# Performance work log

Measured on AMD Instinct MI355X. Metric: run time of the kernel, lower is better.

Reference implementation:

```python
import jax, jax.numpy as jnp
import numpy as np

N_NODES = 100000
N_EDGES = 1600000
D_IN = 128
D_OUT = 128


def setup_inputs() -> dict:
    key = jax.random.key(0)
    k1, k2, k3, k4 = jax.random.split(key, 4)
    feat = jax.random.normal(k1, (N_NODES, D_IN), dtype=jnp.float32)
    W1 = jax.random.normal(k2, (D_OUT, D_IN), dtype=jnp.float32) * (1.0 / np.sqrt(D_IN))
    src = jax.random.randint(k3, (N_EDGES,), 0, N_NODES, dtype=jnp.int32)
    # ensure every dst node has at least one in-edge (no empty segments, like a
    # DGL graph without isolated destination nodes)
    dst_rand = jax.random.randint(k4, (N_EDGES - N_NODES,), 0, N_NODES, dtype=jnp.int32)
    dst = jnp.concatenate([jnp.arange(N_NODES, dtype=jnp.int32), dst_rand])
    return {"feat": feat, "W1": W1, "src": src, "dst": dst}


def reference(feat, W1, src, dst):
    # nn.Linear(bias=False): h = feat @ W1.T   -> [N, D_OUT]
    norm_h = jnp.einsum("nd,od->no", feat, W1)
    # copy_u message + max reduce: segment-max of projected src feats onto dst
    msgs = norm_h[src]                                   # [E, D_OUT] gather
    h_N = jax.ops.segment_max(msgs, dst, num_segments=feat.shape[0])  # [N, D_OUT]
    # concat(feat_dst, h_N) along feature dim
    return jnp.concatenate([feat, h_N], axis=1)          # [N, D_IN + D_OUT]
```

## Files before the change

kernel.cpp:

```cpp
#include <hip/hip_runtime.h>
#include <hip/hip_bf16.h>
#include <cfloat>

typedef short bf16x8 __attribute__((ext_vector_type(8)));
typedef float f32x4 __attribute__((ext_vector_type(4)));

constexpr int NB_PAD  = 800;
constexpr int PCHUNK  = 8192;
constexpr int NCH_MAX = 200;
constexpr int OFFROW  = 804;
constexpr int BCAPM   = 4096;

__device__ __forceinline__ unsigned short f32_to_bf16_rne(float f) {
    unsigned int u = __float_as_uint(f);
    u += 0x7fffu + ((u >> 16) & 1u);
    return (unsigned short)(u >> 16);
}
__device__ __forceinline__ float b2f(unsigned int w, int k) {
    return (float)((int)(w << (24 - 8 * k)) >> 24);
}

__global__ __launch_bounds__(256) void ka_part_gemm_kernel(
    const float* __restrict__ feat, const float* __restrict__ W1,
    signed char* __restrict__ norm8, float* __restrict__ rowscale,
    float* __restrict__ out,
    const int* __restrict__ src, const int* __restrict__ dst,
    int* __restrict__ part, unsigned short* __restrict__ offRow,
    int N, int E, int nb, int partBlocks) {
    __shared__ __align__(16) char smem[38912];
    const int t = threadIdx.x;

    if ((int)blockIdx.x < partBlocks) {
        int* stage   = (int*)smem;
        int* pkCnt   = stage + PCHUNK;
        int* pkOff   = pkCnt + 400;
        int* pkLoc   = pkOff + 400;
        int* partial = pkLoc + 400;

        const int c0 = blockIdx.x * PCHUNK;
        const int n  = (E - c0 < PCHUNK) ? (E - c0) : PCHUNK;

        for (int i = t; i < 400; i += 256) pkCnt[i] = 0;
        __syncthreads();

#pragma unroll
        for (int j = 0; j < PCHUNK / 1024; ++j) {
            int i = (j * 256 + t) * 4;
            if (i + 3 < n) {
                int4 d4 = *(const int4*)(dst + c0 + i);
                atomicAdd(&pkCnt[(d4.x >> 7) >> 1], 1 << (((d4.x >> 7) & 1) << 4));
                atomicAdd(&pkCnt[(d4.y >> 7) >> 1], 1 << (((d4.y >> 7) & 1) << 4));
                atomicAdd(&pkCnt[(d4.z >> 7) >> 1], 1 << (((d4.z >> 7) & 1) << 4));
                atomicAdd(&pkCnt[(d4.w >> 7) >> 1], 1 << (((d4.w >> 7) & 1) << 4));
            } else if (i < n) {
                for (int k = i; k < n; ++k) {
                    int b = dst[c0 + k] >> 7;
                    atomicAdd(&pkCnt[b >> 1], 1 << ((b & 1) << 4));
                }
            }
        }
        __syncthreads();

        {
            int w0 = 0, w1 = 0;
            if (t < 200) { w0 = pkCnt[2 * t]; w1 = pkCnt[2 * t + 1]; }
            int c0_ = w0 & 0xFFFF, c1_ = (w0 >> 16) & 0xFFFF;
            int c2_ = w1 & 0xFFFF, c3_ = (w1 >> 16) & 0xFFFF;
            partial[t] = c0_ + c1_ + c2_ + c3_;
            __syncthreads();
            for (int d = 1; d < 256; d <<= 1) {
                int x = (t >= d) ? partial[t - d] : 0;
                __syncthreads();
                if (t >= d) partial[t] += x;
                __syncthreads();
            }
            if (t < 200) {
                int run = t ? partial[t - 1] : 0;
                int o0 = run, o1 = o0 + c0_, o2 = o1 + c1_, o3 = o2 + c2_;
                pkOff[2 * t]     = o0 | (o1 << 16);
                pkOff[2 * t + 1] = o2 | (o3 << 16);
                pkLoc[2 * t]     = o0 | (o1 << 16);
                pkLoc[2 * t + 1] = o2 | (o3 << 16);
            }
        }
        __syncthreads();

#pragma unroll
        for (int j = 0; j < PCHUNK / 1024; ++j) {
            int i = (j * 256 + t) * 4;
            if (i + 3 < n) {
                int4 d4 = *(const int4*)(dst + c0 + i);
                int4 s4 = *(const int4*)(src + c0 + i);
                int b, sh, old;
                b = d4.x >> 7; sh = (b & 1) << 4;
                old = atomicAdd(&pkLoc[b >> 1], 1 << sh);
                stage[(old >> sh) & 0xFFFF] = s4.x | ((d4.x & 127) << 17);
                b = d4.y >> 7; sh = (b & 1) << 4;
                old = atomicAdd(&pkLoc[b >> 1], 1 << sh);
                stage[(old >> sh) & 0xFFFF] = s4.y | ((d4.y & 127) << 17);
                b = d4.z >> 7; sh = (b & 1) << 4;
                old = atomicAdd(&pkLoc[b >> 1], 1 << sh);
                stage[(old >> sh) & 0xFFFF] = s4.z | ((d4.z & 127) << 17);
                b = d4.w >> 7; sh = (b & 1) << 4;
                old = atomicAdd(&pkLoc[b >> 1], 1 << sh);
                stage[(old >> sh) & 0xFFFF] = s4.w | ((d4.w & 127) << 17);
            } else if (i < n) {
                for (int k = i; k < n; ++k) {
                    int d = dst[c0 + k];
                    int b = d >> 7, sh = (b & 1) << 4;
                    int old = atomicAdd(&pkLoc[b >> 1], 1 << sh);
                    stage[(old >> sh) & 0xFFFF] = src[c0 + k] | ((d & 127) << 17);
                }
            }
        }
        __syncthreads();

        for (int i = t * 4; i < n; i += 1024) {
            if (i + 3 < n) *(int4*)(part + c0 + i) = *(const int4*)(stage + i);
            else for (int k = i; k < n; ++k) part[c0 + k] = stage[k];
        }
        unsigned short* orow = offRow + (size_t)blockIdx.x * OFFROW;
        for (int b = t; b <= nb; b += 256)
            orow[b] = (unsigned short)((pkOff[b >> 1] >> ((b & 1) << 4)) & 0xFFFF);
    } else {
        unsigned short* smW = (unsigned short*)smem;
#pragma unroll
        for (int i = 0; i < 8; ++i) {
            int f = i * 256 + t;
            int l = f & 63, kb = (f >> 6) & 3, ot = f >> 8;
            int wrow = ot * 16 + (l & 15);
            int k0 = kb * 32 + (l >> 4) * 8;
            const float* p = W1 + wrow * 128 + k0;
            float4 f0 = *(const float4*)p;
            float4 f1 = *(const float4*)(p + 4);
            union { unsigned short h[8]; uint4 v; } pk;
            pk.h[0] = f32_to_bf16_rne(f0.x); pk.h[1] = f32_to_bf16_rne(f0.y);
            pk.h[2] = f32_to_bf16_rne(f0.z); pk.h[3] = f32_to_bf16_rne(f0.w);
            pk.h[4] = f32_to_bf16_rne(f1.x); pk.h[5] = f32_to_bf16_rne(f1.y);
            pk.h[6] = f32_to_bf16_rne(f1.z); pk.h[7] = f32_to_bf16_rne(f1.w);
            *(uint4*)(smW + (size_t)f * 8) = pk.v;
        }

        const int bid = blockIdx.x - partBlocks;
        const int w = t >> 6;
        const int l = t & 63;
        const int brow0 = bid * 64;
        const int row = brow0 + w * 16 + (l & 15);
        const int kq = (l >> 4) * 8;
        const bool valid = row < N;

        bf16x8 a[4];
        const float* fr = feat + (size_t)row * 128;
        float* orow_ = out + (size_t)row * 256;
#pragma unroll
        for (int kb = 0; kb < 4; ++kb) {
            float4 f0 = make_float4(0.f, 0.f, 0.f, 0.f), f1 = f0;
            if (valid) {
                f0 = *(const float4*)(fr + kb * 32 + kq);
                f1 = *(const float4*)(fr + kb * 32 + kq + 4);
                *(float4*)(orow_ + kb * 32 + kq) = f0;
                *(float4*)(orow_ + kb * 32 + kq + 4) = f1;
            }
            bf16x8 av;
            av[0] = (short)f32_to_bf16_rne(f0.x); av[1] = (short)f32_to_bf16_rne(f0.y);
            av[2] = (short)f32_to_bf16_rne(f0.z); av[3] = (short)f32_to_bf16_rne(f0.w);
            av[4] = (short)f32_to_bf16_rne(f1.x); av[5] = (short)f32_to_bf16_rne(f1.y);
            av[6] = (short)f32_to_bf16_rne(f1.z); av[7] = (short)f32_to_bf16_rne(f1.w);
            a[kb] = av;
        }
        __syncthreads();

        const bf16x8* bfr = (const bf16x8*)smem;
        f32x4 zero = {0.f, 0.f, 0.f, 0.f};
        f32x4 acc[8];
#pragma unroll
        for (int ot = 0; ot < 8; ++ot) acc[ot] = zero;
#pragma unroll
        for (int ot = 0; ot < 8; ++ot) {
#pragma unroll
            for (int kb = 0; kb < 4; ++kb) {
                bf16x8 b = bfr[(ot * 4 + kb) * 64 + l];
                acc[ot] = __builtin_amdgcn_mfma_f32_16x16x32_bf16(a[kb], b, acc[ot], 0, 0, 0);
            }
        }

        const int r0 = w * 16 + (l >> 4) * 4;
        float inv[4], scl[4];
#pragma unroll
        for (int j = 0; j < 4; ++j) {
            float am = 0.f;
#pragma unroll
            for (int ot = 0; ot < 8; ++ot) am = fmaxf(am, __builtin_fabsf(acc[ot][j]));
#pragma unroll
            for (int d = 1; d < 16; d <<= 1) am = fmaxf(am, __shfl_xor(am, d, 64));
            am = fmaxf(am, 1e-30f);
            inv[j] = 127.0f / am;
            scl[j] = am * (1.0f / 127.0f);
        }
        if ((l & 15) == 0) {
#pragma unroll
            for (int j = 0; j < 4; ++j) {
                int grow = brow0 + r0 + j;
                if (grow < N) rowscale[grow] = scl[j];
            }
        }
        __syncthreads();

        char (*sm8)[144] = (char (*)[144])smem;
        const int c0 = l & 15;
#pragma unroll
        for (int ot = 0; ot < 8; ++ot)
#pragma unroll
            for (int j = 0; j < 4; ++j)
                sm8[r0 + j][ot * 16 + c0] = (char)(int)rintf(acc[ot][j] * inv[j]);
        __syncthreads();
#pragma unroll
        for (int i = 0; i < 2; ++i) {
            int idx = i * 256 + t;
            int r = idx >> 3, c = idx & 7;
            int grow = brow0 + r;
            if (grow < N) {
                uint4 v = *(const uint4*)&sm8[r][c * 16];
                *(uint4*)(norm8 + (size_t)grow * 128 + c * 16) = v;
            }
        }
    }
}

__global__ __launch_bounds__(512) void kb_maxpool_kernel(
    const signed char* __restrict__ norm8, const float* __restrict__ rowscale,
    const int* __restrict__ part, const unsigned short* __restrict__ offRow,
    float* __restrict__ out, int N, int nch) {
    __shared__ int eraw[BCAPM];
    __shared__ int esrc[BCAPM];
    __shared__ int runs_s[NCH_MAX];
    __shared__ int rlen[NCH_MAX + 1];
    __shared__ int eoff[129];
    __shared__ int eloc[128];
    __shared__ int s128[128];

    const int B = blockIdx.x;
    const int t = threadIdx.x;

    for (int c = t; c < nch; c += 512) {
        const unsigned short* orow = offRow + (size_t)c * OFFROW;
        int s = orow[B];
        int e = orow[B + 1];
        runs_s[c] = s;
        rlen[c] = e - s;
    }
    __syncthreads();
    if (t < 64) {
        int carry = 0;
        int rounds = (nch + 63) / 64;
        for (int r = 0; r < rounds; ++r) {
            int c = r * 64 + t;
            int orig = (c < nch) ? rlen[c] : 0;
            int v = orig;
#pragma unroll
            for (int d = 1; d < 64; d <<= 1) {
                int x = __shfl_up(v, d, 64);
                if (t >= d) v += x;
            }
            if (c < nch) rlen[c] = carry + v - orig;
            carry += __shfl(v, 63, 64);
        }
        if (t == 0) rlen[nch] = carry;
    }
    __syncthreads();
    int cnt = rlen[nch];
    if (cnt > BCAPM) cnt = BCAPM;

    {
        int g = t >> 4, ln = t & 15;
        for (int c = g; c < nch; c += 32) {
            int s = runs_s[c], d0 = rlen[c], l = rlen[c + 1] - rlen[c];
            const int* gp = part + (size_t)c * PCHUNK + s;
            for (int i = ln; i < l; i += 16) {
                int d = d0 + i;
                if (d < BCAPM) eraw[d] = gp[i];
            }
        }
    }
    if (t < 128) eloc[t] = 0;
    __syncthreads();

    for (int i = t; i < cnt; i += 512) atomicAdd(&eloc[eraw[i] >> 17], 1);
    __syncthreads();
    if (t < 128) s128[t] = eloc[t];
    __syncthreads();
    for (int d = 1; d < 128; d <<= 1) {
        int x = 0;
        if (t < 128 && t >= d) x = s128[t - d];
        __syncthreads();
        if (t < 128 && t >= d) s128[t] += x;
        __syncthreads();
    }
    if (t < 128) {
        int e = t ? s128[t - 1] : 0;
        eoff[t] = e;
        eloc[t] = e;
    }
    if (t == 0) eoff[128] = cnt;
    __syncthreads();
    for (int i = t; i < cnt; i += 512) {
        int v = eraw[i];
        esrc[atomicAdd(&eloc[v >> 17], 1)] = v & 0x1FFFF;
    }
    __syncthreads();

    int qw = t >> 4;
    int ln = t & 15;
    const size_t colb = (size_t)ln * 8;
    for (int dl = qw; dl < 128; dl += 32) {
        int node = (B << 7) + dl;
        if (node >= N) break;
        int si = eoff[dl], se = eoff[dl + 1];
        if (se > BCAPM) se = BCAPM;
        float a0 = -FLT_MAX, a1 = -FLT_MAX, a2 = -FLT_MAX, a3 = -FLT_MAX;
        float a4 = -FLT_MAX, a5 = -FLT_MAX, a6 = -FLT_MAX, a7 = -FLT_MAX;
        float b0 = -FLT_MAX, b1 = -FLT_MAX, b2 = -FLT_MAX, b3 = -FLT_MAX;
        float b4 = -FLT_MAX, b5 = -FLT_MAX, b6 = -FLT_MAX, b7 = -FLT_MAX;
        float c0 = -FLT_MAX, c1 = -FLT_MAX, c2 = -FLT_MAX, c3 = -FLT_MAX;
        float c4 = -FLT_MAX, c5 = -FLT_MAX, c6 = -FLT_MAX, c7 = -FLT_MAX;
        float d0 = -FLT_MAX, d1 = -FLT_MAX, d2 = -FLT_MAX, d3 = -FLT_MAX;
        float d4 = -FLT_MAX, d5 = -FLT_MAX, d6 = -FLT_MAX, d7 = -FLT_MAX;
        int i = si;
        for (; i + 3 < se; i += 4) {
            int s1 = esrc[i], s2 = esrc[i + 1], s3 = esrc[i + 2], s4 = esrc[i + 3];
            uint2 wA = *(const uint2*)(norm8 + (size_t)s1 * 128 + colb);
            uint2 wB = *(const uint2*)(norm8 + (size_t)s2 * 128 + colb);
            uint2 wC = *(const uint2*)(norm8 + (size_t)s3 * 128 + colb);
            uint2 wD = *(const uint2*)(norm8 + (size_t)s4 * 128 + colb);
            float sA = rowscale[s1], sB = rowscale[s2];
            float sC = rowscale[s3], sD = rowscale[s4];
            a0 = fmaxf(a0, b2f(wA.x, 0) * sA); a1 = fmaxf(a1, b2f(wA.x, 1) * sA);
            a2 = fmaxf(a2, b2f(wA.x, 2) * sA); a3 = fmaxf(a3, b2f(wA.x, 3) * sA);
            a4 = fmaxf(a4, b2f(wA.y, 0) * sA); a5 = fmaxf(a5, b2f(wA.y, 1) * sA);
            a6 = fmaxf(a6, b2f(wA.y, 2) * sA); a7 = fmaxf(a7, b2f(wA.y, 3) * sA);
            b0 = fmaxf(b0, b2f(wB.x, 0) * sB); b1 = fmaxf(b1, b2f(wB.x, 1) * sB);
            b2 = fmaxf(b2, b2f(wB.x, 2) * sB); b3 = fmaxf(b3, b2f(wB.x, 3) * sB);
            b4 = fmaxf(b4, b2f(wB.y, 0) * sB); b5 = fmaxf(b5, b2f(wB.y, 1) * sB);
            b6 = fmaxf(b6, b2f(wB.y, 2) * sB); b7 = fmaxf(b7, b2f(wB.y, 3) * sB);
            c0 = fmaxf(c0, b2f(wC.x, 0) * sC); c1 = fmaxf(c1, b2f(wC.x, 1) * sC);
            c2 = fmaxf(c2, b2f(wC.x, 2) * sC); c3 = fmaxf(c3, b2f(wC.x, 3) * sC);
            c4 = fmaxf(c4, b2f(wC.y, 0) * sC); c5 = fmaxf(c5, b2f(wC.y, 1) * sC);
            c6 = fmaxf(c6, b2f(wC.y, 2) * sC); c7 = fmaxf(c7, b2f(wC.y, 3) * sC);
            d0 = fmaxf(d0, b2f(wD.x, 0) * sD); d1 = fmaxf(d1, b2f(wD.x, 1) * sD);
            d2 = fmaxf(d2, b2f(wD.x, 2) * sD); d3 = fmaxf(d3, b2f(wD.x, 3) * sD);
            d4 = fmaxf(d4, b2f(wD.y, 0) * sD); d5 = fmaxf(d5, b2f(wD.y, 1) * sD);
            d6 = fmaxf(d6, b2f(wD.y, 2) * sD); d7 = fmaxf(d7, b2f(wD.y, 3) * sD);
        }
        for (; i < se; ++i) {
            int s1 = esrc[i];
            uint2 wA = *(const uint2*)(norm8 + (size_t)s1 * 128 + colb);
            float sA = rowscale[s1];
            a0 = fmaxf(a0, b2f(wA.x, 0) * sA); a1 = fmaxf(a1, b2f(wA.x, 1) * sA);
            a2 = fmaxf(a2, b2f(wA.x, 2) * sA); a3 = fmaxf(a3, b2f(wA.x, 3) * sA);
            a4 = fmaxf(a4, b2f(wA.y, 0) * sA); a5 = fmaxf(a5, b2f(wA.y, 1) * sA);
            a6 = fmaxf(a6, b2f(wA.y, 2) * sA); a7 = fmaxf(a7, b2f(wA.y, 3) * sA);
        }
        a0 = fmaxf(a0, b0); a1 = fmaxf(a1, b1); a2 = fmaxf(a2, b2); a3 = fmaxf(a3, b3);
        a4 = fmaxf(a4, b4); a5 = fmaxf(a5, b5); a6 = fmaxf(a6, b6); a7 = fmaxf(a7, b7);
        c0 = fmaxf(c0, d0); c1 = fmaxf(c1, d1); c2 = fmaxf(c2, d2); c3 = fmaxf(c3, d3);
        c4 = fmaxf(c4, d4); c5 = fmaxf(c5, d5); c6 = fmaxf(c6, d6); c7 = fmaxf(c7, d7);
        a0 = fmaxf(a0, c0); a1 = fmaxf(a1, c1); a2 = fmaxf(a2, c2); a3 = fmaxf(a3, c3);
        a4 = fmaxf(a4, c4); a5 = fmaxf(a5, c5); a6 = fmaxf(a6, c6); a7 = fmaxf(a7, c7);
        float* op = out + (size_t)node * 256 + 128 + colb;
        *(float4*)op       = make_float4(a0, a1, a2, a3);
        *(float4*)(op + 4) = make_float4(a4, a5, a6, a7);
    }
}

extern "C" void kernel_launch(void* const* d_in, const int* in_sizes, int n_in,
                              void* d_out, int out_size, void* d_ws, size_t ws_size,
                              hipStream_t stream) {
    const float* feat = (const float*)d_in[0];
    const float* W1   = (const float*)d_in[1];
    const int*   src  = (const int*)d_in[2];
    const int*   dst  = (const int*)d_in[3];
    float* out = (float*)d_out;

    const int N = in_sizes[0] / 128;
    const int E = in_sizes[2];
    const int nb = (N + 127) >> 7;
    const int nchunks = (E + PCHUNK - 1) / PCHUNK;
    const int gemmBlocks = (N + 63) / 64;

    char* wsp = (char*)d_ws;
    size_t o = 0;
    signed char* norm8 = (signed char*)(wsp + o);
    o += ((size_t)N * 128 + 255) & ~(size_t)255;
    float* rowscale = (float*)(wsp + o);
    o += ((size_t)N * 4 + 255) & ~(size_t)255;
    int* part = (int*)(wsp + o);
    o += ((size_t)E * 4 + 255) & ~(size_t)255;
    unsigned short* offRow = (unsigned short*)(wsp + o);
    o += ((size_t)nchunks * OFFROW * 2 + 255) & ~(size_t)255;

    ka_part_gemm_kernel<<<nchunks + gemmBlocks, 256, 0, stream>>>(
        feat, W1, norm8, rowscale, out, src, dst, part, offRow,
        N, E, nb, nchunks);
    kb_maxpool_kernel<<<nb, 512, 0, stream>>>(
        norm8, rowscale, part, offRow, out, N, nchunks);
}
```

Baseline: 95.83 us.

## Halve destination bucket size to 64 nodes with smaller partition chunks

Destination nodes are now bucketed 64 at a time instead of 128, and partition chunks shrink from 8192 to 6144 edges. The max-pool kernel runs with 256 threads per block over twice as many blocks, with less shared memory per block. The in-bucket prefix scan now uses wavefront shuffles instead of a shared-memory scan with repeated barriers. The aim is more parallelism and occupancy in the gather phase, at the cost of more chunk rows each pool block must read and more bucket counters per partition block.

```diff
diff --git a/kernel.cpp b/kernel.cpp
--- a/kernel.cpp
+++ b/kernel.cpp
@@ -5,11 +5,11 @@
 typedef short bf16x8 __attribute__((ext_vector_type(8)));
 typedef float f32x4 __attribute__((ext_vector_type(4)));
 
-constexpr int NB_PAD  = 800;
-constexpr int PCHUNK  = 8192;
-constexpr int NCH_MAX = 200;
-constexpr int OFFROW  = 804;
-constexpr int BCAPM   = 4096;
+constexpr int NB2     = 1600;
+constexpr int PCHUNK  = 6144;
+constexpr int NCH_MAX = 264;
+constexpr int OFFROW  = 1604;
+constexpr int BCAPK   = 2048;
 
 __device__ __forceinline__ unsigned short f32_to_bf16_rne(float f) {
     unsigned int u = __float_as_uint(f);
@@ -26,21 +26,21 @@
     float* __restrict__ out,
     const int* __restrict__ src, const int* __restrict__ dst,
     int* __restrict__ part, unsigned short* __restrict__ offRow,
-    int N, int E, int nb, int partBlocks) {
-    __shared__ __align__(16) char smem[38912];
+    int N, int E, int partBlocks) {
+    __shared__ __align__(16) char smem[35200];
     const int t = threadIdx.x;
 
     if ((int)blockIdx.x < partBlocks) {
         int* stage   = (int*)smem;
         int* pkCnt   = stage + PCHUNK;
-        int* pkOff   = pkCnt + 400;
-        int* pkLoc   = pkOff + 400;
-        int* partial = pkLoc + 400;
+        int* pkOff   = pkCnt + 800;
+        int* pkLoc   = pkOff + 800;
+        int* partial = pkLoc + 800;
 
         const int c0 = blockIdx.x * PCHUNK;
         const int n  = (E - c0 < PCHUNK) ? (E - c0) : PCHUNK;
 
-        for (int i = t; i < 400; i += 256) pkCnt[i] = 0;
+        for (int i = t; i < 800; i += 256) pkCnt[i] = 0;
         __syncthreads();
 
 #pragma unroll
@@ -48,13 +48,13 @@
             int i = (j * 256 + t) * 4;
             if (i + 3 < n) {
                 int4 d4 = *(const int4*)(dst + c0 + i);
-                atomicAdd(&pkCnt[(d4.x >> 7) >> 1], 1 << (((d4.x >> 7) & 1) << 4));
-                atomicAdd(&pkCnt[(d4.y >> 7) >> 1], 1 << (((d4.y >> 7) & 1) << 4));
-                atomicAdd(&pkCnt[(d4.z >> 7) >> 1], 1 << (((d4.z >> 7) & 1) << 4));
-                atomicAdd(&pkCnt[(d4.w >> 7) >> 1], 1 << (((d4.w >> 7) & 1) << 4));
+                atomicAdd(&pkCnt[(d4.x >> 6) >> 1], 1 << (((d4.x >> 6) & 1) << 4));
+                atomicAdd(&pkCnt[(d4.y >> 6) >> 1], 1 << (((d4.y >> 6) & 1) << 4));
+                atomicAdd(&pkCnt[(d4.z >> 6) >> 1], 1 << (((d4.z >> 6) & 1) << 4));
+                atomicAdd(&pkCnt[(d4.w >> 6) >> 1], 1 << (((d4.w >> 6) & 1) << 4));
             } else if (i < n) {
                 for (int k = i; k < n; ++k) {
-                    int b = dst[c0 + k] >> 7;
+                    int b = dst[c0 + k] >> 6;
                     atomicAdd(&pkCnt[b >> 1], 1 << ((b & 1) << 4));
                 }
             }
@@ -62,11 +62,16 @@
         __syncthreads();
 
         {
-            int w0 = 0, w1 = 0;
-            if (t < 200) { w0 = pkCnt[2 * t]; w1 = pkCnt[2 * t + 1]; }
-            int c0_ = w0 & 0xFFFF, c1_ = (w0 >> 16) & 0xFFFF;
-            int c2_ = w1 & 0xFFFF, c3_ = (w1 >> 16) & 0xFFFF;
-            partial[t] = c0_ + c1_ + c2_ + c3_;
+            int w0 = 0, w1 = 0, w2 = 0, w3 = 0;
+            if (t < 200) {
+                w0 = pkCnt[4 * t];     w1 = pkCnt[4 * t + 1];
+                w2 = pkCnt[4 * t + 2]; w3 = pkCnt[4 * t + 3];
+            }
+            int cA = w0 & 0xFFFF, cB = (w0 >> 16) & 0xFFFF;
+            int cC = w1 & 0xFFFF, cD = (w1 >> 16) & 0xFFFF;
+            int cE = w2 & 0xFFFF, cF = (w2 >> 16) & 0xFFFF;
+            int cG = w3 & 0xFFFF, cH = (w3 >> 16) & 0xFFFF;
+            partial[t] = cA + cB + cC + cD + cE + cF + cG + cH;
             __syncthreads();
             for (int d = 1; d < 256; d <<= 1) {
                 int x = (t >= d) ? partial[t - d] : 0;
@@ -76,11 +81,16 @@
             }
             if (t < 200) {
                 int run = t ? partial[t - 1] : 0;
-                int o0 = run, o1 = o0 + c0_, o2 = o1 + c1_, o3 = o2 + c2_;
-                pkOff[2 * t]     = o0 | (o1 << 16);
-                pkOff[2 * t + 1] = o2 | (o3 << 16);
-                pkLoc[2 * t]     = o0 | (o1 << 16);
-                pkLoc[2 * t + 1] = o2 | (o3 << 16);
+                int o0 = run,      o1 = o0 + cA, o2 = o1 + cB, o3 = o2 + cC;
+                int o4 = o3 + cD,  o5 = o4 + cE, o6 = o5 + cF, o7 = o6 + cG;
+                pkOff[4 * t]     = o0 | (o1 << 16);
+                pkOff[4 * t + 1] = o2 | (o3 << 16);
+                pkOff[4 * t + 2] = o4 | (o5 << 16);
+                pkOff[4 * t + 3] = o6 | (o7 << 16);
+                pkLoc[4 * t]     = o0 | (o1 << 16);
+                pkLoc[4 * t + 1] = o2 | (o3 << 16);
+                pkLoc[4 * t + 2] = o4 | (o5 << 16);
+                pkLoc[4 * t + 3] = o6 | (o7 << 16);
             }
         }
         __syncthreads();
@@ -92,24 +102,24 @@
                 int4 d4 = *(const int4*)(dst + c0 + i);
                 int4 s4 = *(const int4*)(src + c0 + i);
                 int b, sh, old;
-                b = d4.x >> 7; sh = (b & 1) << 4;
+                b = d4.x >> 6; sh = (b & 1) << 4;
                 old = atomicAdd(&pkLoc[b >> 1], 1 << sh);
-                stage[(old >> sh) & 0xFFFF] = s4.x | ((d4.x & 127) << 17);
-                b = d4.y >> 7; sh = (b & 1) << 4;
+                stage[(old >> sh) & 0xFFFF] = s4.x | ((d4.x & 63) << 17);
+                b = d4.y >> 6; sh = (b & 1) << 4;
                 old = atomicAdd(&pkLoc[b >> 1], 1 << sh);
-                stage[(old >> sh) & 0xFFFF] = s4.y | ((d4.y & 127) << 17);
-                b = d4.z >> 7; sh = (b & 1) << 4;
+                stage[(old >> sh) & 0xFFFF] = s4.y | ((d4.y & 63) << 17);
+                b = d4.z >> 6; sh = (b & 1) << 4;
                 old = atomicAdd(&pkLoc[b >> 1], 1 << sh);
-                stage[(old >> sh) & 0xFFFF] = s4.z | ((d4.z & 127) << 17);
-                b = d4.w >> 7; sh = (b & 1) << 4;
+                stage[(old >> sh) & 0xFFFF] = s4.z | ((d4.z & 63) << 17);
+                b = d4.w >> 6; sh = (b & 1) << 4;
                 old = atomicAdd(&pkLoc[b >> 1], 1 << sh);
-                stage[(old >> sh) & 0xFFFF] = s4.w | ((d4.w & 127) << 17);
+                stage[(old >> sh) & 0xFFFF] = s4.w | ((d4.w & 63) << 17);
             } else if (i < n) {
                 for (int k = i; k < n; ++k) {
                     int d = dst[c0 + k];
-                    int b = d >> 7, sh = (b & 1) << 4;
+                    int b = d >> 6, sh = (b & 1) << 4;
                     int old = atomicAdd(&pkLoc[b >> 1], 1 << sh);
-                    stage[(old >> sh) & 0xFFFF] = src[c0 + k] | ((d & 127) << 17);
+                    stage[(old >> sh) & 0xFFFF] = src[c0 + k] | ((d & 63) << 17);
                 }
             }
         }
@@ -120,8 +130,10 @@
             else for (int k = i; k < n; ++k) part[c0 + k] = stage[k];
         }
         unsigned short* orow = offRow + (size_t)blockIdx.x * OFFROW;
-        for (int b = t; b <= nb; b += 256)
-            orow[b] = (unsigned short)((pkOff[b >> 1] >> ((b & 1) << 4)) & 0xFFFF);
+        for (int b = t; b <= NB2; b += 256) {
+            int v = (b < NB2) ? ((pkOff[b >> 1] >> ((b & 1) << 4)) & 0xFFFF) : n;
+            orow[b] = (unsigned short)v;
+        }
     } else {
         unsigned short* smW = (unsigned short*)smem;
 #pragma unroll
@@ -227,28 +239,28 @@
     }
 }
 
-__global__ __launch_bounds__(512) void kb_maxpool_kernel(
+__global__ __launch_bounds__(256) void kb_maxpool_kernel(
     const signed char* __restrict__ norm8, const float* __restrict__ rowscale,
     const int* __restrict__ part, const unsigned short* __restrict__ offRow,
     float* __restrict__ out, int N, int nch) {
-    __shared__ int eraw[BCAPM];
-    __shared__ int esrc[BCAPM];
+    __shared__ int eraw[BCAPK];
+    __shared__ int esrc[BCAPK];
     __shared__ int runs_s[NCH_MAX];
     __shared__ int rlen[NCH_MAX + 1];
-    __shared__ int eoff[129];
-    __shared__ int eloc[128];
-    __shared__ int s128[128];
+    __shared__ int eoff[65];
+    __shared__ int eloc[64];
 
     const int B = blockIdx.x;
     const int t = threadIdx.x;
 
-    for (int c = t; c < nch; c += 512) {
+    for (int c = t; c < nch; c += 256) {
         const unsigned short* orow = offRow + (size_t)c * OFFROW;
         int s = orow[B];
         int e = orow[B + 1];
         runs_s[c] = s;
         rlen[c] = e - s;
     }
+    if (t < 64) eloc[t] = 0;
     __syncthreads();
     if (t < 64) {
         int carry = 0;
@@ -269,41 +281,38 @@
     }
     __syncthreads();
     int cnt = rlen[nch];
-    if (cnt > BCAPM) cnt = BCAPM;
+    if (cnt > BCAPK) cnt = BCAPK;
 
     {
         int g = t >> 4, ln = t & 15;
-        for (int c = g; c < nch; c += 32) {
+        for (int c = g; c < nch; c += 16) {
             int s = runs_s[c], d0 = rlen[c], l = rlen[c + 1] - rlen[c];
             const int* gp = part + (size_t)c * PCHUNK + s;
             for (int i = ln; i < l; i += 16) {
                 int d = d0 + i;
-                if (d < BCAPM) eraw[d] = gp[i];
-            }
-        }
-    }
-    if (t < 128) eloc[t] = 0;
-    __syncthreads();
-
-    for (int i = t; i < cnt; i += 512) atomicAdd(&eloc[eraw[i] >> 17], 1);
-    __syncthreads();
-    if (t < 128) s128[t] = eloc[t];
-    __syncthreads();
-    for (int d = 1; d < 128; d <<= 1) {
-        int x = 0;
-        if (t < 128 && t >= d) x = s128[t - d];
-        __syncthreads();
-        if (t < 128 && t >= d) s128[t] += x;
-        __syncthreads();
-    }
-    if (t < 128) {
-        int e = t ? s128[t - 1] : 0;
-        eoff[t] = e;
-        eloc[t] = e;
-    }
-    if (t == 0) eoff[128] = cnt;
-    __syncthreads();
-    for (int i = t; i < cnt; i += 512) {
+                if (d < BCAPK) eraw[d] = gp[i];
+            }
+        }
+    }
+    __syncthreads();
+
+    for (int i = t; i < cnt; i += 256) atomicAdd(&eloc[eraw[i] >> 17], 1);
+    __syncthreads();
+    if (t < 64) {
+        int v = eloc[t];
+        int sc = v;
+#pragma unroll
+        for (int d = 1; d < 64; d <<= 1) {
+            int x = __shfl_up(sc, d, 64);
+            if (t >= d) sc += x;
+        }
+        int excl = sc - v;
+        eoff[t] = excl;
+        eloc[t] = excl;
+        if (t == 63) eoff[64] = sc;
+    }
+    __syncthreads();
+    for (int i = t; i < cnt; i += 256) {
         int v = eraw[i];
         esrc[atomicAdd(&eloc[v >> 17], 1)] = v & 0x1FFFF;
     }
@@ -312,11 +321,11 @@
     int qw = t >> 4;
     int ln = t & 15;
     const size_t colb = (size_t)ln * 8;
-    for (int dl = qw; dl < 128; dl += 32) {
-        int node = (B << 7) + dl;
+    for (int dl = qw; dl < 64; dl += 16) {
+        int node = (B << 6) + dl;
         if (node >= N) break;
         int si = eoff[dl], se = eoff[dl + 1];
-        if (se > BCAPM) se = BCAPM;
+        if (se > BCAPK) se = BCAPK;
         float a0 = -FLT_MAX, a1 = -FLT_MAX, a2 = -FLT_MAX, a3 = -FLT_MAX;
         float a4 = -FLT_MAX, a5 = -FLT_MAX, a6 = -FLT_MAX, a7 = -FLT_MAX;
         float b0 = -FLT_MAX, b1 = -FLT_MAX, b2 = -FLT_MAX, b3 = -FLT_MAX;
@@ -383,7 +392,7 @@
 
     const int N = in_sizes[0] / 128;
     const int E = in_sizes[2];
-    const int nb = (N + 127) >> 7;
+    const int nbk = (N + 63) >> 6;
     const int nchunks = (E + PCHUNK - 1) / PCHUNK;
     const int gemmBlocks = (N + 63) / 64;
 
@@ -400,7 +409,7 @@
 
     ka_part_gemm_kernel<<<nchunks + gemmBlocks, 256, 0, stream>>>(
         feat, W1, norm8, rowscale, out, src, dst, part, offRow,
-        N, E, nb, nchunks);
-    kb_maxpool_kernel<<<nb, 512, 0, stream>>>(
+        N, E, nchunks);
+    kb_maxpool_kernel<<<nbk, 256, 0, stream>>>(
         norm8, rowscale, part, offRow, out, N, nchunks);
 }
```

Measured after the change: 97.96 us. 2.2% more time.
